# Optimization experiments

Hardware: AMD Instinct MI355X
Metric: run time of the kernel (lower is better)

Reference implementation:

```python
import jax, jax.numpy as jnp
import numpy as np
from math import sqrt

B, L, D_MODEL = 4, 128, 256
V, D_WORD = 50257, 768
H = 8  # n_heads; d_keys = D_MODEL // H = 32


def setup_inputs() -> dict:
    key = jax.random.key(0)
    ks = jax.random.split(key, 10)
    s = lambda k, shape, fan: jax.random.normal(k, shape, dtype=jnp.float32) / np.sqrt(fan)
    return {
        "time_series_embedding": jax.random.normal(ks[0], (B, L, D_MODEL), dtype=jnp.float32),
        "word_embedding": jax.random.normal(ks[1], (V, D_WORD), dtype=jnp.float32) * 0.02,
        "Wq": s(ks[2], (D_MODEL, D_MODEL), D_MODEL),
        "bq": jnp.zeros((D_MODEL,), jnp.float32),
        "Wk": s(ks[3], (D_WORD, D_MODEL), D_WORD),
        "bk": jnp.zeros((D_MODEL,), jnp.float32),
        "Wv": s(ks[4], (D_WORD, D_MODEL), D_WORD),
        "bv": jnp.zeros((D_MODEL,), jnp.float32),
        "Wo": s(ks[5], (D_MODEL, D_MODEL), D_MODEL),
        "bo": jnp.zeros((D_MODEL,), jnp.float32),
    }


def reference(time_series_embedding, word_embedding, Wq, bq, Wk, bk, Wv, bv, Wo, bo):
    b, l, _ = time_series_embedding.shape
    v, _ = word_embedding.shape
    h = H
    e = D_MODEL // h
    # projections
    query = (time_series_embedding @ Wq + bq).reshape(b, l, h, e)   # [B,L,H,E]
    key = (word_embedding @ Wk + bk).reshape(v, h, e)               # [V,H,E]
    value = (word_embedding @ Wv + bv).reshape(v, h, e)             # [V,H,E]
    scale = 1.0 / sqrt(e)
    # scores over full vocab: [B,H,V,L]
    scores = jnp.einsum('blhe,vhe->bhvl', query, key)
    # NOTE: faithful to source -- softmax over the LAST axis (l, the query dim)
    attn = jax.nn.softmax(scale * scores, axis=-1)
    # dropout is identity in eval mode
    reprog = jnp.einsum('bhvl,vhe->blhe', attn, value).reshape(b, l, h * e)
    return reprog @ Wo + bo  # [B,L,d_model]
```

## Files before the change

### kernel.cpp

```cpp
#include <hip/hip_runtime.h>
#include <hip/hip_bf16.h>
#include <string.h>

#define BB 4
#define LL 128
#define DM 256
#define VV 50257
#define VPAD 50304
#define DW 768
#define HH 8
#define EE 32

typedef __attribute__((ext_vector_type(8))) short sh8;
typedef __attribute__((ext_vector_type(4))) short sh4;
typedef __attribute__((ext_vector_type(4))) float f32x4;

static __device__ inline unsigned short bfbits(float x) {
  __hip_bfloat16 h = __float2bfloat16(x);
  unsigned short u;
  __builtin_memcpy(&u, &h, 2);
  return u;
}

#define GLDS16(gsrc, ldst)                                                    \
  __builtin_amdgcn_global_load_lds(                                          \
      (const __attribute__((address_space(1))) void*)(gsrc),                 \
      (__attribute__((address_space(3))) void*)(ldst), 16, 0, 0)

__global__ __launch_bounds__(256) void qproj_kernel(
    const float* __restrict__ tse, const float* __restrict__ Wq,
    const float* __restrict__ bq, unsigned short* __restrict__ Qb) {
  __shared__ float row[DM];
  int r = blockIdx.x;
  int n = threadIdx.x;
  row[n] = tse[r * DM + n];
  __syncthreads();
  float acc = bq[n];
#pragma unroll 8
  for (int k = 0; k < DM; ++k)
    acc = fmaf(row[k], Wq[k * DM + n], acc);
  const float scale = 0.17677669529663687f * 1.4426950408889634f;
  Qb[r * DM + n] = bfbits(acc * scale);
}

__global__ __launch_bounds__(256) void wtrans_kernel(
    const float* __restrict__ Wk, const float* __restrict__ Wv,
    unsigned short* __restrict__ Wkt, unsigned short* __restrict__ Wvt) {
  __shared__ float tileS[64][65];
  const float* src = blockIdx.z ? Wv : Wk;
  unsigned short* dst = blockIdx.z ? Wvt : Wkt;
  int k0 = blockIdx.x * 64, n0 = blockIdx.y * 64;
  int t = threadIdx.x;
  int c = t & 63, rb = t >> 6;
#pragma unroll
  for (int j = 0; j < 16; ++j) {
    int r = j * 4 + rb;
    tileS[r][c] = src[(size_t)(k0 + r) * DM + n0 + c];
  }
  __syncthreads();
#pragma unroll
  for (int j = 0; j < 16; ++j) {
    int r = j * 4 + rb;
    dst[(size_t)(n0 + r) * DW + k0 + c] = bfbits(tileS[c][r]);
  }
}

__global__ __launch_bounds__(256, 2) void kvproj_kernel(
    const float* __restrict__ WE, const unsigned short* __restrict__ Wkt,
    const unsigned short* __restrict__ Wvt, const float* __restrict__ bk,
    const float* __restrict__ bv, unsigned short* __restrict__ Kb,
    unsigned short* __restrict__ Vb) {
  __shared__ float WEf[2][128 * 32];
  __shared__ short Kbuf[2][128 * 32];
  __shared__ short Vbuf[2][128 * 32];

  int bx = blockIdx.x;
  int v0 = (bx >> 1) * 128;
  int colbase = (bx & 1) * 128;
  int t = threadIdx.x;
  int w = t >> 6, lane = t & 63, a = lane & 15, quad = lane >> 4;
  int wm = w >> 1, wn = w & 1;

  auto stage = [&](int kt, int p) {
#pragma unroll
    for (int i = 0; i < 4; ++i) {
      int s = w * 256 + i * 64 + lane;
      int row = s >> 3;
      int cc = (s & 7) ^ (row & 7);
      int grow = v0 + row;
      if (grow > VV - 1) grow = VV - 1;
      GLDS16(WE + (size_t)grow * DW + kt * 32 + cc * 4,
             &WEf[p][(w * 256 + i * 64) * 4]);
    }
#pragma unroll
    for (int i = 0; i < 2; ++i) {
      int s = w * 128 + i * 64 + lane;
      int row = s >> 2, cc = s & 3;
      GLDS16(Wkt + (size_t)(colbase + row) * DW + kt * 32 + cc * 8,
             &Kbuf[p][(w * 128 + i * 64) * 8]);
      GLDS16(Wvt + (size_t)(colbase + row) * DW + kt * 32 + cc * 8,
             &Vbuf[p][(w * 128 + i * 64) * 8]);
    }
  };

  f32x4 Ck[4][4], Cv[4][4];
#pragma unroll
  for (int mb = 0; mb < 4; ++mb)
#pragma unroll
    for (int nb = 0; nb < 4; ++nb) {
      Ck[mb][nb] = (f32x4){0.f, 0.f, 0.f, 0.f};
      Cv[mb][nb] = (f32x4){0.f, 0.f, 0.f, 0.f};
    }

  stage(0, 0);
  __syncthreads();

  for (int kt = 0; kt < 24; ++kt) {
    int p = kt & 1;
    if (kt < 23) stage(kt + 1, p ^ 1);

    sh8 A[4], Bk[4], Bv[4];
#pragma unroll
    for (int mb = 0; mb < 4; ++mb) {
      int row = wm * 64 + mb * 16 + a;
      const float* rp = &WEf[p][row * 32];
      f32x4 lo = *(const f32x4*)(rp + ((2 * quad) ^ (a & 7)) * 4);
      f32x4 hi = *(const f32x4*)(rp + ((2 * quad + 1) ^ (a & 7)) * 4);
      sh4 l4 = {(short)bfbits(lo[0]), (short)bfbits(lo[1]),
                (short)bfbits(lo[2]), (short)bfbits(lo[3])};
      sh4 h4 = {(short)bfbits(hi[0]), (short)bfbits(hi[1]),
                (short)bfbits(hi[2]), (short)bfbits(hi[3])};
      A[mb] = __builtin_shufflevector(l4, h4, 0, 1, 2, 3, 4, 5, 6, 7);
    }
#pragma unroll
    for (int nb = 0; nb < 4; ++nb) {
      Bk[nb] = *(const sh8*)&Kbuf[p][((wn * 4 + nb) * 16 + a) * 32 + quad * 8];
      Bv[nb] = *(const sh8*)&Vbuf[p][((wn * 4 + nb) * 16 + a) * 32 + quad * 8];
    }
#pragma unroll
    for (int mb = 0; mb < 4; ++mb)
#pragma unroll
      for (int nb = 0; nb < 4; ++nb) {
        Ck[mb][nb] = __builtin_amdgcn_mfma_f32_16x16x32_bf16(
            A[mb], Bk[nb], Ck[mb][nb], 0, 0, 0);
        Cv[mb][nb] = __builtin_amdgcn_mfma_f32_16x16x32_bf16(
            A[mb], Bv[nb], Cv[mb][nb], 0, 0, 0);
      }
    __syncthreads();
  }

  float bkv[4], bvv[4];
#pragma unroll
  for (int nb = 0; nb < 4; ++nb) {
    int n = colbase + (wn * 4 + nb) * 16 + a;
    bkv[nb] = bk[n];
    bvv[nb] = bv[n];
  }
#pragma unroll
  for (int mb = 0; mb < 4; ++mb)
#pragma unroll
    for (int nb = 0; nb < 4; ++nb)
#pragma unroll
      for (int r = 0; r < 4; ++r) {
        int m = v0 + wm * 64 + mb * 16 + quad * 4 + r;
        int n = colbase + (wn * 4 + nb) * 16 + a;
        bool ok = m < VV;
        Kb[(size_t)m * DM + n] = ok ? bfbits(Ck[mb][nb][r] + bkv[nb]) : 0;
        Vb[(size_t)m * DM + n] = ok ? bfbits(Cv[mb][nb][r] + bvv[nb]) : 0;
      }
}

#define PST 72
__global__ __launch_bounds__(256) void attn_kernel(
    const unsigned short* __restrict__ Qb, const unsigned short* __restrict__ Kb,
    const unsigned short* __restrict__ Vb, float* __restrict__ part, int bpb,
    int nc) {
  __shared__ short Pb[LL * PST];
  __shared__ short Vt[EE * PST];

  int bh = blockIdx.x / bpb;
  int chunk = blockIdx.x - bh * bpb;
  int b = bh >> 3, h = bh & 7;
  int t = threadIdx.x;
  int w = t >> 6;
  int lane = t & 63;
  int a = lane & 15;
  int quad = lane >> 4;
  int vr = t >> 2, e0 = (t & 3) * 8;

  sh8 qf[8];
  const unsigned short* qbase = Qb + (size_t)(b * LL) * DM + h * EE;
#pragma unroll
  for (int tau = 0; tau < 8; ++tau)
    qf[tau] = *(const sh8*)(qbase + (size_t)(tau * 16 + a) * DM + quad * 8);

  f32x4 C[2][2];
#pragma unroll
  for (int mb = 0; mb < 2; ++mb)
#pragma unroll
    for (int nb = 0; nb < 2; ++nb)
      C[mb][nb] = (f32x4){0.f, 0.f, 0.f, 0.f};

  const int ntiles = VPAD >> 6;

  sh8 af, vv;
  {
    int v0 = chunk << 6;
    af = *(const sh8*)(Kb + (size_t)(v0 + 16 * w + a) * DM + h * EE + quad * 8);
    vv = *(const sh8*)(Vb + (size_t)(v0 + vr) * DM + h * EE + e0);
  }

  for (int tile = chunk; tile < ntiles; tile += bpb) {
    f32x4 S[8];
#pragma unroll
    for (int tau = 0; tau < 8; ++tau) {
      f32x4 z = {0.f, 0.f, 0.f, 0.f};
      S[tau] = __builtin_amdgcn_mfma_f32_16x16x32_bf16(af, qf[tau], z, 0, 0, 0);
    }

    float sm[4], inv[4];
#pragma unroll
    for (int r = 0; r < 4; ++r) sm[r] = 0.f;
#pragma unroll
    for (int tau = 0; tau < 8; ++tau)
#pragma unroll
      for (int r = 0; r < 4; ++r) {
        float ex = __builtin_amdgcn_exp2f(S[tau][r]);
        S[tau][r] = ex;
        sm[r] += ex;
      }
#pragma unroll
    for (int msk = 1; msk <= 8; msk <<= 1)
#pragma unroll
      for (int r = 0; r < 4; ++r)
        sm[r] += __shfl_xor(sm[r], msk);
#pragma unroll
    for (int r = 0; r < 4; ++r) inv[r] = 1.f / sm[r];

    __syncthreads();

    {
      const short* vs = (const short*)&vv;
#pragma unroll
      for (int j = 0; j < 8; ++j)
        Vt[(e0 + j) * PST + vr] = vs[j];
    }
#pragma unroll
    for (int tau = 0; tau < 8; ++tau) {
      ushort4 pk;
      pk.x = bfbits(S[tau][0] * inv[0]);
      pk.y = bfbits(S[tau][1] * inv[1]);
      pk.z = bfbits(S[tau][2] * inv[2]);
      pk.w = bfbits(S[tau][3] * inv[3]);
      *(ushort4*)&Pb[(tau * 16 + a) * PST + 16 * w + quad * 4] = pk;
    }
    __syncthreads();

    int nt = tile + bpb;
    if (nt < ntiles) {
      int v0n = nt << 6;
      af = *(const sh8*)(Kb + (size_t)(v0n + 16 * w + a) * DM + h * EE + quad * 8);
      vv = *(const sh8*)(Vb + (size_t)(v0n + vr) * DM + h * EE + e0);
    }

    sh8 Afr[2][2], Bfr[2][2];
#pragma unroll
    for (int mb = 0; mb < 2; ++mb)
#pragma unroll
      for (int kb = 0; kb < 2; ++kb)
        Afr[mb][kb] =
            *(const sh8*)&Pb[(32 * w + mb * 16 + a) * PST + kb * 32 + quad * 8];
#pragma unroll
    for (int kb = 0; kb < 2; ++kb)
#pragma unroll
      for (int nb = 0; nb < 2; ++nb)
        Bfr[kb][nb] = *(const sh8*)&Vt[(nb * 16 + a) * PST + kb * 32 + quad * 8];
#pragma unroll
    for (int kb = 0; kb < 2; ++kb)
#pragma unroll
      for (int mb = 0; mb < 2; ++mb)
#pragma unroll
        for (int nb = 0; nb < 2; ++nb)
          C[mb][nb] = __builtin_amdgcn_mfma_f32_16x16x32_bf16(
              Afr[mb][kb], Bfr[kb][nb], C[mb][nb], 0, 0, 0);
  }

#pragma unroll
  for (int mb = 0; mb < 2; ++mb)
#pragma unroll
    for (int nb = 0; nb < 2; ++nb)
#pragma unroll
      for (int r = 0; r < 4; ++r) {
        int l = 32 * w + mb * 16 + quad * 4 + r;
        int e = nb * 16 + a;
        size_t idx = (size_t)(b * LL + l) * DM + h * EE + e;
        if (nc > 1)
          part[(size_t)chunk * (BB * LL * DM) + idx] = C[mb][nb][r];
        else
          atomicAdd(&part[idx], C[mb][nb][r]);
      }
}

__global__ __launch_bounds__(256) void outproj_kernel(
    const float* __restrict__ part, const float* __restrict__ Wo,
    const float* __restrict__ bo, float* __restrict__ out, int nc) {
  __shared__ float row[DM];
  int r = blockIdx.x, n = threadIdx.x;
  float s = 0.f;
  for (int c = 0; c < nc; ++c)
    s += part[(size_t)c * (BB * LL * DM) + (size_t)r * DM + n];
  row[n] = s;
  __syncthreads();
  float acc = bo[n];
#pragma unroll 8
  for (int k = 0; k < DM; ++k)
    acc = fmaf(row[k], Wo[k * DM + n], acc);
  out[r * DM + n] = acc;
}

extern "C" void kernel_launch(void* const* d_in, const int* in_sizes, int n_in,
                              void* d_out, int out_size, void* d_ws, size_t ws_size,
                              hipStream_t stream) {
  const float* tse = (const float*)d_in[0];
  const float* WE  = (const float*)d_in[1];
  const float* Wq  = (const float*)d_in[2];
  const float* bq  = (const float*)d_in[3];
  const float* Wk  = (const float*)d_in[4];
  const float* bk  = (const float*)d_in[5];
  const float* Wv  = (const float*)d_in[6];
  const float* bv  = (const float*)d_in[7];
  const float* Wo  = (const float*)d_in[8];
  const float* bo  = (const float*)d_in[9];
  float* out = (float*)d_out;

  char* ws = (char*)d_ws;
  const size_t QB_BYTES   = (size_t)BB * LL * DM * 2;
  const size_t KV_BYTES   = (size_t)VPAD * DM * 2;
  const size_t WT_BYTES   = (size_t)DM * DW * 2;
  const size_t PART_BYTES = (size_t)BB * LL * DM * 4;
  unsigned short* Qb  = (unsigned short*)ws;
  unsigned short* Kb  = (unsigned short*)(ws + QB_BYTES);
  unsigned short* Vb  = (unsigned short*)(ws + QB_BYTES + KV_BYTES);
  char* X = ws + QB_BYTES + 2 * KV_BYTES;
  unsigned short* Wkt = (unsigned short*)X;
  unsigned short* Wvt = (unsigned short*)(X + WT_BYTES);
  float* part = (float*)X;

  const int BPB = 32;

  const size_t NEED_PART =
      QB_BYTES + 2 * KV_BYTES + (size_t)BPB * PART_BYTES;
  const int nc = (ws_size >= NEED_PART) ? BPB : 1;

  wtrans_kernel<<<dim3(DW / 64, DM / 64, 2), 256, 0, stream>>>(Wk, Wv, Wkt, Wvt);
  qproj_kernel<<<BB * LL, 256, 0, stream>>>(tse, Wq, bq, Qb);
  kvproj_kernel<<<(VPAD / 128) * 2, 256, 0, stream>>>(WE, Wkt, Wvt, bk, bv, Kb, Vb);
  if (nc == 1)
    (void)hipMemsetAsync(part, 0, PART_BYTES, stream);
  attn_kernel<<<32 * BPB, 256, 0, stream>>>(Qb, Kb, Vb, part, BPB, nc);
  outproj_kernel<<<BB * LL, 256, 0, stream>>>(part, Wo, bo, out, nc);
}
```

Measured before the change: 426.0 us.

## Merge prep kernels, deepen KV-projection prefetch, swizzle LDS, hoist attention loads

Merges the weight-transpose and Q-projection kernels into one launch to save a kernel launch. In the KV-projection GEMM, the global-to-LDS staging now runs two tiles ahead, with explicit vmcnt waits and raw barriers, and the K/V weight tiles in LDS are XOR-swizzled to cut bank conflicts. In the attention kernel, the next tile's K/V global loads are issued before the softmax, so their latency overlaps the exp work. Hand-placed waitcnt and sched_barrier calls add a risk of ordering mistakes, and the double-buffer reuse has to match the wait counts exactly.

```diff
diff --git a/kernel.cpp b/kernel.cpp
--- a/kernel.cpp
+++ b/kernel.cpp
@@ -27,41 +27,51 @@
       (const __attribute__((address_space(1))) void*)(gsrc),                 \
       (__attribute__((address_space(3))) void*)(ldst), 16, 0, 0)
 
-__global__ __launch_bounds__(256) void qproj_kernel(
+#define WAIT_VM(N)                                                           \
+  asm volatile("s_waitcnt vmcnt(" #N ")" ::: "memory");                      \
+  __builtin_amdgcn_sched_barrier(0)
+#define WAIT_LGKM0                                                           \
+  asm volatile("s_waitcnt lgkmcnt(0)" ::: "memory");                         \
+  __builtin_amdgcn_sched_barrier(0)
+
+__global__ __launch_bounds__(256) void prep_kernel(
+    const float* __restrict__ Wk, const float* __restrict__ Wv,
+    unsigned short* __restrict__ Wkt, unsigned short* __restrict__ Wvt,
     const float* __restrict__ tse, const float* __restrict__ Wq,
     const float* __restrict__ bq, unsigned short* __restrict__ Qb) {
-  __shared__ float row[DM];
-  int r = blockIdx.x;
-  int n = threadIdx.x;
-  row[n] = tse[r * DM + n];
-  __syncthreads();
-  float acc = bq[n];
+  __shared__ float tileS[64][65];
+  int bid = blockIdx.x;
+  int t = threadIdx.x;
+  if (bid < 96) {
+    int z = bid / 48, rem = bid - z * 48;
+    int x = rem % 12, y = rem / 12;
+    const float* src = z ? Wv : Wk;
+    unsigned short* dst = z ? Wvt : Wkt;
+    int k0 = x * 64, n0 = y * 64;
+    int c = t & 63, rb = t >> 6;
+#pragma unroll
+    for (int j = 0; j < 16; ++j) {
+      int r = j * 4 + rb;
+      tileS[r][c] = src[(size_t)(k0 + r) * DM + n0 + c];
+    }
+    __syncthreads();
+#pragma unroll
+    for (int j = 0; j < 16; ++j) {
+      int r = j * 4 + rb;
+      dst[(size_t)(n0 + r) * DW + k0 + c] = bfbits(tileS[c][r]);
+    }
+  } else {
+    int r = bid - 96;
+    int n = t;
+    float* row = &tileS[0][0];
+    row[n] = tse[r * DM + n];
+    __syncthreads();
+    float acc = bq[n];
 #pragma unroll 8
-  for (int k = 0; k < DM; ++k)
-    acc = fmaf(row[k], Wq[k * DM + n], acc);
-  const float scale = 0.17677669529663687f * 1.4426950408889634f;
-  Qb[r * DM + n] = bfbits(acc * scale);
-}
-
-__global__ __launch_bounds__(256) void wtrans_kernel(
-    const float* __restrict__ Wk, const float* __restrict__ Wv,
-    unsigned short* __restrict__ Wkt, unsigned short* __restrict__ Wvt) {
-  __shared__ float tileS[64][65];
-  const float* src = blockIdx.z ? Wv : Wk;
-  unsigned short* dst = blockIdx.z ? Wvt : Wkt;
-  int k0 = blockIdx.x * 64, n0 = blockIdx.y * 64;
-  int t = threadIdx.x;
-  int c = t & 63, rb = t >> 6;
-#pragma unroll
-  for (int j = 0; j < 16; ++j) {
-    int r = j * 4 + rb;
-    tileS[r][c] = src[(size_t)(k0 + r) * DM + n0 + c];
-  }
-  __syncthreads();
-#pragma unroll
-  for (int j = 0; j < 16; ++j) {
-    int r = j * 4 + rb;
-    dst[(size_t)(n0 + r) * DW + k0 + c] = bfbits(tileS[c][r]);
+    for (int k = 0; k < DM; ++k)
+      acc = fmaf(row[k], Wq[k * DM + n], acc);
+    const float scale = 0.17677669529663687f * 1.4426950408889634f;
+    Qb[r * DM + n] = bfbits(acc * scale);
   }
 }
 
@@ -95,7 +105,8 @@
 #pragma unroll
     for (int i = 0; i < 2; ++i) {
       int s = w * 128 + i * 64 + lane;
-      int row = s >> 2, cc = s & 3;
+      int row = s >> 2;
+      int cc = (s & 3) ^ ((row >> 1) & 3);
       GLDS16(Wkt + (size_t)(colbase + row) * DW + kt * 32 + cc * 8,
              &Kbuf[p][(w * 128 + i * 64) * 8]);
       GLDS16(Wvt + (size_t)(colbase + row) * DW + kt * 32 + cc * 8,
@@ -113,11 +124,17 @@
     }
 
   stage(0, 0);
-  __syncthreads();
+  stage(1, 1);
 
   for (int kt = 0; kt < 24; ++kt) {
     int p = kt & 1;
-    if (kt < 23) stage(kt + 1, p ^ 1);
+    if (kt < 23) {
+      WAIT_VM(8);
+    } else {
+      WAIT_VM(0);
+    }
+    __builtin_amdgcn_s_barrier();
+    __builtin_amdgcn_sched_barrier(0);
 
     sh8 A[4], Bk[4], Bv[4];
 #pragma unroll
@@ -134,8 +151,10 @@
     }
 #pragma unroll
     for (int nb = 0; nb < 4; ++nb) {
-      Bk[nb] = *(const sh8*)&Kbuf[p][((wn * 4 + nb) * 16 + a) * 32 + quad * 8];
-      Bv[nb] = *(const sh8*)&Vbuf[p][((wn * 4 + nb) * 16 + a) * 32 + quad * 8];
+      int krow = (wn * 4 + nb) * 16 + a;
+      int cp = (quad ^ ((krow >> 1) & 3)) * 8;
+      Bk[nb] = *(const sh8*)&Kbuf[p][krow * 32 + cp];
+      Bv[nb] = *(const sh8*)&Vbuf[p][krow * 32 + cp];
     }
 #pragma unroll
     for (int mb = 0; mb < 4; ++mb)
@@ -146,7 +165,11 @@
         Cv[mb][nb] = __builtin_amdgcn_mfma_f32_16x16x32_bf16(
             A[mb], Bv[nb], Cv[mb][nb], 0, 0, 0);
       }
-    __syncthreads();
+
+    WAIT_LGKM0;
+    __builtin_amdgcn_s_barrier();
+    __builtin_amdgcn_sched_barrier(0);
+    if (kt < 22) stage(kt + 2, p);
   }
 
   float bkv[4], bvv[4];
@@ -218,6 +241,14 @@
       S[tau] = __builtin_amdgcn_mfma_f32_16x16x32_bf16(af, qf[tau], z, 0, 0, 0);
     }
 
+    sh8 af2 = af, vv2 = vv;
+    int nt = tile + bpb;
+    if (nt < ntiles) {
+      int v0n = nt << 6;
+      af2 = *(const sh8*)(Kb + (size_t)(v0n + 16 * w + a) * DM + h * EE + quad * 8);
+      vv2 = *(const sh8*)(Vb + (size_t)(v0n + vr) * DM + h * EE + e0);
+    }
+
     float sm[4], inv[4];
 #pragma unroll
     for (int r = 0; r < 4; ++r) sm[r] = 0.f;
@@ -237,7 +268,9 @@
 #pragma unroll
     for (int r = 0; r < 4; ++r) inv[r] = 1.f / sm[r];
 
-    __syncthreads();
+    WAIT_LGKM0;
+    __builtin_amdgcn_s_barrier();
+    __builtin_amdgcn_sched_barrier(0);
 
     {
       const short* vs = (const short*)&vv;
@@ -254,14 +287,12 @@
       pk.w = bfbits(S[tau][3] * inv[3]);
       *(ushort4*)&Pb[(tau * 16 + a) * PST + 16 * w + quad * 4] = pk;
     }
-    __syncthreads();
-
-    int nt = tile + bpb;
-    if (nt < ntiles) {
-      int v0n = nt << 6;
-      af = *(const sh8*)(Kb + (size_t)(v0n + 16 * w + a) * DM + h * EE + quad * 8);
-      vv = *(const sh8*)(Vb + (size_t)(v0n + vr) * DM + h * EE + e0);
-    }
+    WAIT_LGKM0;
+    __builtin_amdgcn_s_barrier();
+    __builtin_amdgcn_sched_barrier(0);
+
+    af = af2;
+    vv = vv2;
 
     sh8 Afr[2][2], Bfr[2][2];
 #pragma unroll
@@ -352,8 +383,7 @@
       QB_BYTES + 2 * KV_BYTES + (size_t)BPB * PART_BYTES;
   const int nc = (ws_size >= NEED_PART) ? BPB : 1;
 
-  wtrans_kernel<<<dim3(DW / 64, DM / 64, 2), 256, 0, stream>>>(Wk, Wv, Wkt, Wvt);
-  qproj_kernel<<<BB * LL, 256, 0, stream>>>(tse, Wq, bq, Qb);
+  prep_kernel<<<96 + BB * LL, 256, 0, stream>>>(Wk, Wv, Wkt, Wvt, tse, Wq, bq, Qb);
   kvproj_kernel<<<(VPAD / 128) * 2, 256, 0, stream>>>(WE, Wkt, Wvt, bk, bv, Kb, Vb);
   if (nc == 1)
     (void)hipMemsetAsync(part, 0, PART_BYTES, stream);
```

Measured after the change: 401.4 us. -5.8%, faster.
